# Optimization experiments

Measured on AMD Instinct MI355X. Metric: run time of the kernel, lower is better.

## Reference

```python
import jax, jax.numpy as jnp
import numpy as np

N_NODES = 100000
N_EDGES = 1600000
IN_CH = 64
HID = 64
N_GRAPHS = 64


def _sage_conv(x, src, dst, Wl, bl, Wr, n_nodes):
    # PyG SAGEConv (aggr='mean'): out = lin_l(mean_{j in N(i)} x_j) + lin_r(x_i)
    msg = x[src]                                            # [E, d] gather
    agg = jax.ops.segment_sum(msg, dst, num_segments=n_nodes)
    cnt = jax.ops.segment_sum(jnp.ones((src.shape[0],), x.dtype), dst,
                              num_segments=n_nodes)
    agg = agg / jnp.maximum(cnt, 1.0)[:, None]
    return agg @ Wl + bl + x @ Wr


def setup_inputs() -> dict:
    key = jax.random.key(0)
    ks = jax.random.split(key, 16)
    x = jax.random.normal(ks[0], (N_NODES, IN_CH), jnp.float32)
    edge_index = jax.random.randint(ks[1], (2, N_EDGES), 0, N_NODES, jnp.int64)
    batch = jnp.sort(jax.random.randint(ks[2], (N_NODES,), 0, N_GRAPHS, jnp.int64))

    def glorot(k, fan_in, fan_out):
        s = jnp.sqrt(2.0 / (fan_in + fan_out))
        return jax.random.normal(k, (fan_in, fan_out), jnp.float32) * s

    params = {
        'W1l': glorot(ks[3], IN_CH, HID), 'b1': jnp.zeros((HID,), jnp.float32),
        'W1r': glorot(ks[4], IN_CH, HID),
        'W2l': glorot(ks[5], HID, HID), 'b2': jnp.zeros((HID,), jnp.float32),
        'W2r': glorot(ks[6], HID, HID),
        'W3l': glorot(ks[7], HID, HID), 'b3': jnp.zeros((HID,), jnp.float32),
        'W3r': glorot(ks[8], HID, HID),
        'Wc1': glorot(ks[9], HID, HID // 2), 'bc1': jnp.zeros((HID // 2,), jnp.float32),
        'Wc2': glorot(ks[10], HID // 2, 2), 'bc2': jnp.zeros((2,), jnp.float32),
    }
    return {'x': x, 'edge_index': edge_index, 'batch': batch, **params}


def reference(x, edge_index, batch,
              W1l, b1, W1r, W2l, b2, W2r, W3l, b3, W3r,
              Wc1, bc1, Wc2, bc2):
    src, dst = edge_index[0], edge_index[1]
    n = x.shape[0]
    h = jax.nn.relu(_sage_conv(x, src, dst, W1l, b1, W1r, n))   # dropout = identity (eval)
    h = jax.nn.relu(_sage_conv(h, src, dst, W2l, b2, W2r, n))
    h = jax.nn.relu(_sage_conv(h, src, dst, W3l, b3, W3r, n))
    # global mean pool over graphs
    sums = jax.ops.segment_sum(h, batch, num_segments=N_GRAPHS)
    cnts = jax.ops.segment_sum(jnp.ones((n,), h.dtype), batch, num_segments=N_GRAPHS)
    g = sums / jnp.maximum(cnts, 1.0)[:, None]                  # [G, HID]
    # MLP head (dropout = identity at eval)
    return jax.nn.relu(g @ Wc1 + bc1) @ Wc2 + bc2               # [G, 2]
```

## Files before the change

kernel.cpp:

```cpp
#include <hip/hip_runtime.h>
#include <hip/hip_bf16.h>
#include <hip/hip_fp16.h>

typedef unsigned int u32;
typedef unsigned short u16;
typedef _Float16 f16x8 __attribute__((ext_vector_type(8)));
typedef float f32x4 __attribute__((ext_vector_type(4)));

#define NBLK1 512
#define CVTBLK 256
#define MMBLK 256

__device__ __forceinline__ u16 f2h(float f) { return __half_as_ushort(__float2half(f)); }
__device__ __forceinline__ u32 packh2(float a, float b) {
    return (u32)f2h(a) | ((u32)f2h(b) << 16);
}

__device__ __forceinline__ int gidx(const void* p, long long i, int w64) {
    if (w64) return (int)((const long long*)p)[i];
    return ((const int*)p)[i];
}

__device__ __forceinline__ int detect_w64(const int* edge_words, int E, int tid, int* sh) {
    if (tid == 0) *sh = 0;
    __syncthreads();
    const long long totalWords = 2LL * E;
    const long long step = totalWords / 256;
    long long w = ((long long)tid * step) | 1;
    int nz = (w < totalWords) ? edge_words[w] : 0;
    if (nz) atomicOr(sh, 1);
    __syncthreads();
    return (*sh) ? 0 : 1;
}

__global__ void __launch_bounds__(256) fused_hist_cvt(
        const void* __restrict__ edge, int* __restrict__ flag, u32* __restrict__ ticket,
        u32* __restrict__ HG, int E, int n, int nb1,
        const float* __restrict__ X, u16* __restrict__ Xh) {
    if (blockIdx.x < NBLK1) {
        __shared__ u32 h[256];
        __shared__ int shnz;
        const int tid = threadIdx.x;
        h[tid] = 0;
        const int w64 = detect_w64((const int*)edge, E, tid, &shnz);
        if (blockIdx.x == 0 && tid == 0) { flag[0] = w64; ticket[0] = 0; }
        __syncthreads();
        const int chunk = (E + NBLK1 - 1) / NBLK1;
        const int s = blockIdx.x * chunk;
        const int e = min(s + chunk, E);
        for (int i = s + tid; i < e; i += 256) {
            int d = gidx(edge, (long long)E + i, w64);
            if ((unsigned)d >= (unsigned)n) d = 0;
            atomicAdd(&h[d >> 9], 1);
        }
        __syncthreads();
        for (int b = tid; b < nb1; b += 256) HG[b * NBLK1 + blockIdx.x] = h[b];
        return;
    }
    const long long total4 = (long long)n * 16;
    const long long stride = (long long)CVTBLK * 256;
    long long i = (long long)(blockIdx.x - NBLK1) * 256 + threadIdx.x;
    const float4* X4 = (const float4*)X;
    uint2* O = (uint2*)Xh;
    for (; i < total4; i += stride) {
        float4 v = X4[i];
        uint2 o;
        o.x = packh2(v.x, v.y);
        o.y = packh2(v.z, v.w);
        O[i] = o;
    }
}

__global__ void scanAB(u32* __restrict__ HG, u32* __restrict__ blockSums,
                       u32* __restrict__ SB, u32* __restrict__ ticket, int n) {
    __shared__ u32 ts[256];
    __shared__ int isLast;
    const int ITEMS = 8;
    const int tid = threadIdx.x;
    int base = blockIdx.x * 2048 + tid * ITEMS;
    u32 v[ITEMS];
    u32 sum = 0;
#pragma unroll
    for (int i = 0; i < ITEMS; ++i) {
        int idx = base + i;
        v[i] = (idx < n) ? HG[idx] : 0;
        sum += v[i];
    }
    ts[tid] = sum;
    __syncthreads();
    u32 incl = sum;
    for (int d = 1; d < 256; d <<= 1) {
        u32 y = 0;
        if (tid >= d) y = ts[tid - d];
        __syncthreads();
        incl += y;
        ts[tid] = incl;
        __syncthreads();
    }
    u32 run = incl - sum;
#pragma unroll
    for (int i = 0; i < ITEMS; ++i) {
        int idx = base + i;
        if (idx < n) HG[idx] = run;
        run += v[i];
    }
    if (tid == 255) {
        atomicExch(&blockSums[blockIdx.x], incl);
        __threadfence();
        u32 t = atomicAdd(&ticket[0], 1u);
        isLast = (t == gridDim.x - 1);
    }
    __syncthreads();
    if (!isLast) return;
    const int nb = gridDim.x;
    u32 bv = (tid < nb) ? atomicAdd(&blockSums[tid], 0u) : 0;
    ts[tid] = bv;
    __syncthreads();
    u32 bincl = bv;
    for (int d = 1; d < 256; d <<= 1) {
        u32 y = 0;
        if (tid >= d) y = ts[tid - d];
        __syncthreads();
        bincl += y;
        ts[tid] = bincl;
        __syncthreads();
    }
    if (tid < nb) SB[tid] = bincl - bv;
}

__global__ void __launch_bounds__(256) p1_scatter(const void* __restrict__ edge,
                                                  const int* __restrict__ flag,
                                                  const u32* __restrict__ HG,
                                                  const u32* __restrict__ SB,
                                                  u32* __restrict__ P, int E, int n, int nb1) {
    __shared__ u32 base[256];
    __shared__ u32 cur[256];
    const int tid = threadIdx.x;
    cur[tid] = 0;
    for (int b = tid; b < nb1; b += 256) {
        int i = b * NBLK1 + blockIdx.x;
        base[b] = HG[i] + SB[i >> 11];
    }
    __syncthreads();
    const int w64 = flag[0];
    const int chunk = (E + NBLK1 - 1) / NBLK1;
    const int s = blockIdx.x * chunk;
    const int e = min(s + chunk, E);
    for (int i = s + tid; i < e; i += 256) {
        int d = gidx(edge, (long long)E + i, w64);
        if ((unsigned)d >= (unsigned)n) d = 0;
        int sv = gidx(edge, i, w64);
        if ((unsigned)sv >= (unsigned)n) sv = 0;
        const int b1 = d >> 9;
        u32 r = atomicAdd(&cur[b1], 1);
        P[base[b1] + r] = (u32)sv | ((u32)(d & 511) << 17);
    }
}

__global__ void __launch_bounds__(512) p2_kernel(const u32* __restrict__ P,
                                                 const u32* __restrict__ HG,
                                                 const u32* __restrict__ SB,
                                                 u32* __restrict__ offs,
                                                 int* __restrict__ ss,
                                                 float* __restrict__ pool,
                                                 int E, int n, int nb1) {
    __shared__ u32 h2[512];
    __shared__ u32 ts[512];
    const int tid = threadIdx.x;
    const int b = blockIdx.x;
    if (b == 0)
        for (int i = tid; i < 4096; i += 512) pool[i] = 0.f;
    const int i0 = b * NBLK1;
    const int bs = (int)(HG[i0] + SB[i0 >> 11]);
    int be;
    if (b + 1 < nb1) {
        const int i1 = (b + 1) * NBLK1;
        be = (int)(HG[i1] + SB[i1 >> 11]);
    } else be = E;
    h2[tid] = 0;
    __syncthreads();
    for (int i = bs + tid; i < be; i += 512) atomicAdd(&h2[(P[i] >> 17) & 511], 1);
    __syncthreads();
    u32 v = h2[tid];
    ts[tid] = v;
    __syncthreads();
    u32 incl = v;
    for (int d = 1; d < 512; d <<= 1) {
        u32 y = 0;
        if (tid >= d) y = ts[tid - d];
        __syncthreads();
        incl += y;
        ts[tid] = incl;
        __syncthreads();
    }
    u32 run = incl - v;
    h2[tid] = run;
    const int node0 = b * 512 + tid;
    if (node0 < n) offs[node0] = bs + run;
    if (b == 0 && tid == 0) offs[n] = (u32)E;
    __syncthreads();
    for (int i = bs + tid; i < be; i += 512) {
        u32 p = P[i];
        u32 r = atomicAdd(&h2[(p >> 17) & 511], 1);
        ss[bs + r] = (int)(p & 0x1FFFFu);
    }
}

__global__ void __launch_bounds__(256, 8) agg_kernel(
        const u16* __restrict__ G, const u32* __restrict__ offs,
        const int* __restrict__ ss, u16* __restrict__ M, int n) {
    const int lane = threadIdx.x & 63;
    const int quad = lane >> 4;
    const int m16 = lane & 15;
    const int ntiles = (n + 15) >> 4;
    const int nwaves = gridDim.x * 4;
    for (int tile = blockIdx.x * 4 + (threadIdx.x >> 6); tile < ntiles; tile += nwaves) {
        const int nodeBase = tile << 4;
        const int node_m = nodeBase + m16;
        const int valid = node_m < n;
        const int nodeA = valid ? node_m : n - 1;
        const u32 o0 = offs[nodeA];
        const int deg = valid ? (int)(offs[nodeA + 1] - o0) : 0;
        const int* sp = ss + o0;
        f16x8 s0, s1;
#pragma unroll
        for (int j = 0; j < 8; ++j) { s0[j] = (_Float16)0; s1[j] = (_Float16)0; }
        int e = 0;
        for (; e + 4 <= deg; e += 4) {
            const int iA = sp[e], iB = sp[e + 1], iC = sp[e + 2], iD = sp[e + 3];
            const f16x8* pA = (const f16x8*)(G + ((size_t)iA << 6)) + quad;
            const f16x8* pB = (const f16x8*)(G + ((size_t)iB << 6)) + quad;
            const f16x8* pC = (const f16x8*)(G + ((size_t)iC << 6)) + quad;
            const f16x8* pD = (const f16x8*)(G + ((size_t)iD << 6)) + quad;
            f16x8 a0 = pA[0], a1 = pA[4];
            f16x8 b0 = pB[0], b1 = pB[4];
            f16x8 c0 = pC[0], c1 = pC[4];
            f16x8 d0 = pD[0], d1 = pD[4];
            s0 += a0; s1 += a1;
            s0 += b0; s1 += b1;
            s0 += c0; s1 += c1;
            s0 += d0; s1 += d1;
        }
        for (; e < deg; ++e) {
            const int iA = sp[e];
            const f16x8* pA = (const f16x8*)(G + ((size_t)iA << 6)) + quad;
            s0 += pA[0]; s1 += pA[4];
        }
        const float rdf = deg > 0 ? 1.f / (float)deg : 0.f;
        const _Float16 hrd = (_Float16)rdf;
#pragma unroll
        for (int j = 0; j < 8; ++j) { s0[j] *= hrd; s1[j] *= hrd; }
        if (valid) {
            *(f16x8*)(M + (size_t)node_m * 64 + quad * 8) = s0;
            *(f16x8*)(M + (size_t)node_m * 64 + 32 + quad * 8) = s1;
        }
    }
}

__global__ void __launch_bounds__(256) mm_fused(
        const u16* __restrict__ M, const u16* __restrict__ G,
        const float* __restrict__ Wl, const float* __restrict__ Wr,
        const float* __restrict__ Bv,
        u16* __restrict__ Hout, float* __restrict__ pool,
        const void* __restrict__ batch, const int* __restrict__ flag,
        int n, int mode) {
    const int lane = threadIdx.x & 63;
    const int quad = lane >> 4;
    const int m16 = lane & 15;
    f16x8 bl[2][4], br[2][4];
#pragma unroll
    for (int kh = 0; kh < 2; ++kh)
#pragma unroll
        for (int t = 0; t < 4; ++t)
#pragma unroll
            for (int j = 0; j < 8; ++j) {
                int k = kh * 32 + quad * 8 + j;
                int c = t * 16 + m16;
                bl[kh][t][j] = (_Float16)Wl[k * 64 + c];
                br[kh][t][j] = (_Float16)Wr[k * 64 + c];
            }
    float bias_t[4];
#pragma unroll
    for (int t = 0; t < 4; ++t) bias_t[t] = Bv[t * 16 + m16];
    const int w64 = mode ? flag[0] : 0;

    const int ntiles = (n + 15) >> 4;
    const int nwaves = gridDim.x * 4;
    for (int tile = blockIdx.x * 4 + (threadIdx.x >> 6); tile < ntiles; tile += nwaves) {
        const int nodeBase = tile << 4;
        const int node_m = nodeBase + m16;
        const int nodeA = node_m < n ? node_m : n - 1;
        const f16x8 am0 = *(const f16x8*)(M + (size_t)nodeA * 64 + quad * 8);
        const f16x8 am1 = *(const f16x8*)(M + (size_t)nodeA * 64 + 32 + quad * 8);
        const f16x8 as0 = *(const f16x8*)(G + (size_t)nodeA * 64 + quad * 8);
        const f16x8 as1 = *(const f16x8*)(G + (size_t)nodeA * 64 + 32 + quad * 8);
        f32x4 c[4];
#pragma unroll
        for (int t = 0; t < 4; ++t) {
            f32x4 acc = {bias_t[t], bias_t[t], bias_t[t], bias_t[t]};
            acc = __builtin_amdgcn_mfma_f32_16x16x32_f16(am0, bl[0][t], acc, 0, 0, 0);
            acc = __builtin_amdgcn_mfma_f32_16x16x32_f16(am1, bl[1][t], acc, 0, 0, 0);
            acc = __builtin_amdgcn_mfma_f32_16x16x32_f16(as0, br[0][t], acc, 0, 0, 0);
            acc = __builtin_amdgcn_mfma_f32_16x16x32_f16(as1, br[1][t], acc, 0, 0, 0);
            c[t] = acc;
        }
        if (mode == 0) {
#pragma unroll
            for (int rg = 0; rg < 4; ++rg) {
                const int node = nodeBase + quad * 4 + rg;
                if (node < n) {
#pragma unroll
                    for (int t = 0; t < 4; ++t)
                        Hout[(size_t)node * 64 + t * 16 + m16] = f2h(fmaxf(c[t][rg], 0.f));
                }
            }
        } else {
            float v[4][4];
#pragma unroll
            for (int t = 0; t < 4; ++t)
#pragma unroll
                for (int rg = 0; rg < 4; ++rg) v[t][rg] = fmaxf(c[t][rg], 0.f);
            const int lastN = nodeBase + 15 < n ? nodeBase + 15 : n - 1;
            const int g0 = gidx(batch, nodeBase, w64) & 63;
            const int g1 = gidx(batch, lastN, w64) & 63;
            if (nodeBase + 15 < n && g0 == g1) {
#pragma unroll
                for (int t = 0; t < 4; ++t) {
                    float cs = v[t][0] + v[t][1] + v[t][2] + v[t][3];
                    cs += __shfl_xor(cs, 16, 64);
                    cs += __shfl_xor(cs, 32, 64);
                    if (quad == 0) atomicAdd(&pool[g0 * 64 + t * 16 + m16], cs);
                }
            } else {
#pragma unroll
                for (int rg = 0; rg < 4; ++rg) {
                    const int node = nodeBase + quad * 4 + rg;
                    if (node < n) {
                        const int g = gidx(batch, node, w64) & 63;
#pragma unroll
                        for (int t = 0; t < 4; ++t)
                            atomicAdd(&pool[g * 64 + t * 16 + m16], v[t][rg]);
                    }
                }
            }
        }
    }
}

__global__ void head_kernel(const float* __restrict__ pool, const void* __restrict__ batch,
                            const int* __restrict__ flag,
                            const float* __restrict__ Wc1, const float* __restrict__ bc1,
                            const float* __restrict__ Wc2, const float* __restrict__ bc2,
                            float* __restrict__ out, int n) {
    __shared__ float gm[64 * 64];
    __shared__ float am[64 * 32];
    __shared__ int cnts[64];
    const int tid = threadIdx.x;
    const int w64 = flag[0];
    if (tid < 64) {
        int lo = 0, hi = n;
        while (lo < hi) { int mid = (lo + hi) >> 1; if (gidx(batch, mid, w64) < tid) lo = mid + 1; else hi = mid; }
        int lo2 = 0, hi2 = n;
        int v2 = tid + 1;
        while (lo2 < hi2) { int mid = (lo2 + hi2) >> 1; if (gidx(batch, mid, w64) < v2) lo2 = mid + 1; else hi2 = mid; }
        cnts[tid] = lo2 - lo;
    }
    __syncthreads();
    for (int i = tid; i < 4096; i += 256) {
        int g = i >> 6;
        float c = (float)(cnts[g] > 0 ? cnts[g] : 1);
        gm[i] = pool[i] / c;
    }
    __syncthreads();
    for (int i = tid; i < 64 * 32; i += 256) {
        int g = i >> 5, j = i & 31;
        float acc = bc1[j];
        for (int k = 0; k < 64; ++k) acc += gm[g * 64 + k] * Wc1[k * 32 + j];
        am[i] = acc > 0.f ? acc : 0.f;
    }
    __syncthreads();
    if (tid < 128) {
        int g = tid >> 1, o = tid & 1;
        float acc = bc2[o];
        for (int j = 0; j < 32; ++j) acc += am[g * 32 + j] * Wc2[j * 2 + o];
        out[tid] = acc;
    }
}

extern "C" void kernel_launch(void* const* d_in, const int* in_sizes, int n_in,
                              void* d_out, int out_size, void* d_ws, size_t ws_size,
                              hipStream_t stream) {
    const float* x   = (const float*)d_in[0];
    const void* edge = d_in[1];
    const void* batch = d_in[2];
    const float* W1l = (const float*)d_in[3];
    const float* b1  = (const float*)d_in[4];
    const float* W1r = (const float*)d_in[5];
    const float* W2l = (const float*)d_in[6];
    const float* b2  = (const float*)d_in[7];
    const float* W2r = (const float*)d_in[8];
    const float* W3l = (const float*)d_in[9];
    const float* b3  = (const float*)d_in[10];
    const float* W3r = (const float*)d_in[11];
    const float* Wc1 = (const float*)d_in[12];
    const float* bc1 = (const float*)d_in[13];
    const float* Wc2 = (const float*)d_in[14];
    const float* bc2 = (const float*)d_in[15];

    const int n = in_sizes[0] / 64;
    const int E = in_sizes[1] / 2;
    const int nb1 = (n + 511) >> 9;
    const int NS = nb1 * NBLK1;

    char* w = (char*)d_ws;
    size_t o = 0;
    auto take = [&](size_t bytes) -> void* {
        void* p = w + o;
        o = (o + bytes + 511) & ~(size_t)511;
        return p;
    };
    int* flag      = (int*)take(sizeof(int));
    u32* ticket    = (u32*)take(2 * sizeof(u32));
    u32* offs      = (u32*)take((size_t)(n + 1) * sizeof(u32));
    u32* HG        = (u32*)take((size_t)(NS + 1) * sizeof(u32));
    u32* blockSums = (u32*)take(256 * sizeof(u32));
    u32* SB        = (u32*)take(256 * sizeof(u32));
    u32* P         = (u32*)take((size_t)E * sizeof(u32));
    int* ss        = (int*)take((size_t)E * sizeof(int));
    u16* Xh        = (u16*)take((size_t)n * 64 * sizeof(u16));
    u16* HA        = (u16*)take((size_t)n * 64 * sizeof(u16));
    u16* HB        = (u16*)take((size_t)n * 64 * sizeof(u16));
    u16* M         = (u16*)take((size_t)n * 64 * sizeof(u16));
    float* pool    = (float*)take(64 * 64 * sizeof(float));

    fused_hist_cvt<<<NBLK1 + CVTBLK, 256, 0, stream>>>(edge, flag, ticket, HG, E, n, nb1,
                                                       x, Xh);
    const int nbScan = (NS + 2047) / 2048;
    scanAB<<<nbScan, 256, 0, stream>>>(HG, blockSums, SB, ticket, NS);
    p1_scatter<<<NBLK1, 256, 0, stream>>>(edge, flag, HG, SB, P, E, n, nb1);
    p2_kernel<<<nb1, 512, 0, stream>>>(P, HG, SB, offs, ss, pool, E, n, nb1);

    const int ntiles = (n + 15) >> 4;
    const int AGGBLK = (ntiles + 3) >> 2;
    agg_kernel<<<AGGBLK, 256, 0, stream>>>(Xh, offs, ss, M, n);
    mm_fused<<<MMBLK, 256, 0, stream>>>(M, Xh, W1l, W1r, b1, HA, nullptr, batch, flag, n, 0);
    agg_kernel<<<AGGBLK, 256, 0, stream>>>(HA, offs, ss, M, n);
    mm_fused<<<MMBLK, 256, 0, stream>>>(M, HA, W2l, W2r, b2, HB, nullptr, batch, flag, n, 0);
    agg_kernel<<<AGGBLK, 256, 0, stream>>>(HB, offs, ss, M, n);
    mm_fused<<<MMBLK, 256, 0, stream>>>(M, HB, W3l, W3r, b3, nullptr, pool, batch, flag, n, 1);

    head_kernel<<<1, 256, 0, stream>>>(pool, batch, flag, Wc1, bc1, Wc2, bc2,
                                       (float*)d_out, n);
}
```

Before: 302.1 us.

## Split aggregation into feature slices with edge-parallel lanes and fp32 accumulation

The mean-aggregation kernel is restructured. Each block now handles one of eight 8-channel feature slices, and each node gets four lanes that split its edges among themselves, combining partial sums through xor shuffles. Neighbor indices are prefetched one step ahead and accumulation moves from fp16 to fp32. The grid becomes a fixed persistent size of 8×256 blocks. The aim is better load balance across nodes of differing degree and more parallel gathers in flight. The cost is that each node's index list is read eight times, and each gather is a 16-byte row fragment instead of a wider contiguous load.

```diff
diff --git a/kernel.cpp b/kernel.cpp
--- a/kernel.cpp
+++ b/kernel.cpp
@@ -10,6 +10,7 @@
 #define NBLK1 512
 #define CVTBLK 256
 #define MMBLK 256
+#define AGGBPS 256
 
 __device__ __forceinline__ u16 f2h(float f) { return __half_as_ushort(__float2half(f)); }
 __device__ __forceinline__ u32 packh2(float a, float b) {
@@ -206,53 +207,50 @@
     }
 }
 
-__global__ void __launch_bounds__(256, 8) agg_kernel(
+__global__ void __launch_bounds__(256) agg_kernel(
         const u16* __restrict__ G, const u32* __restrict__ offs,
         const int* __restrict__ ss, u16* __restrict__ M, int n) {
+    const int slice = blockIdx.x & 7;
+    const int blk = blockIdx.x >> 3;
+    const int nblkS = gridDim.x >> 3;
     const int lane = threadIdx.x & 63;
-    const int quad = lane >> 4;
-    const int m16 = lane & 15;
+    const int nsub = lane >> 2;
+    const int e4 = lane & 3;
+
     const int ntiles = (n + 15) >> 4;
-    const int nwaves = gridDim.x * 4;
-    for (int tile = blockIdx.x * 4 + (threadIdx.x >> 6); tile < ntiles; tile += nwaves) {
-        const int nodeBase = tile << 4;
-        const int node_m = nodeBase + m16;
+    const int wavesPerSlice = nblkS * 4;
+    for (int tile = blk * 4 + (threadIdx.x >> 6); tile < ntiles; tile += wavesPerSlice) {
+        const int node_m = (tile << 4) + nsub;
         const int valid = node_m < n;
         const int nodeA = valid ? node_m : n - 1;
         const u32 o0 = offs[nodeA];
         const int deg = valid ? (int)(offs[nodeA + 1] - o0) : 0;
         const int* sp = ss + o0;
-        f16x8 s0, s1;
-#pragma unroll
-        for (int j = 0; j < 8; ++j) { s0[j] = (_Float16)0; s1[j] = (_Float16)0; }
-        int e = 0;
-        for (; e + 4 <= deg; e += 4) {
-            const int iA = sp[e], iB = sp[e + 1], iC = sp[e + 2], iD = sp[e + 3];
-            const f16x8* pA = (const f16x8*)(G + ((size_t)iA << 6)) + quad;
-            const f16x8* pB = (const f16x8*)(G + ((size_t)iB << 6)) + quad;
-            const f16x8* pC = (const f16x8*)(G + ((size_t)iC << 6)) + quad;
-            const f16x8* pD = (const f16x8*)(G + ((size_t)iD << 6)) + quad;
-            f16x8 a0 = pA[0], a1 = pA[4];
-            f16x8 b0 = pB[0], b1 = pB[4];
-            f16x8 c0 = pC[0], c1 = pC[4];
-            f16x8 d0 = pD[0], d1 = pD[4];
-            s0 += a0; s1 += a1;
-            s0 += b0; s1 += b1;
-            s0 += c0; s1 += c1;
-            s0 += d0; s1 += d1;
-        }
-        for (; e < deg; ++e) {
-            const int iA = sp[e];
-            const f16x8* pA = (const f16x8*)(G + ((size_t)iA << 6)) + quad;
-            s0 += pA[0]; s1 += pA[4];
-        }
-        const float rdf = deg > 0 ? 1.f / (float)deg : 0.f;
-        const _Float16 hrd = (_Float16)rdf;
-#pragma unroll
-        for (int j = 0; j < 8; ++j) { s0[j] *= hrd; s1[j] *= hrd; }
-        if (valid) {
-            *(f16x8*)(M + (size_t)node_m * 64 + quad * 8) = s0;
-            *(f16x8*)(M + (size_t)node_m * 64 + 32 + quad * 8) = s1;
+        float acc[8];
+#pragma unroll
+        for (int j = 0; j < 8; ++j) acc[j] = 0.f;
+        int nidx = (e4 < deg) ? sp[e4] : -1;
+        for (int e = 0; e < deg; e += 4) {
+            const int idx = nidx;
+            const int en = e + 4;
+            nidx = (en + e4 < deg) ? sp[en + e4] : -1;
+            if (idx >= 0) {
+                const f16x8 r = *(const f16x8*)(G + ((size_t)idx << 6) + (slice << 3));
+#pragma unroll
+                for (int j = 0; j < 8; ++j) acc[j] += (float)r[j];
+            }
+        }
+#pragma unroll
+        for (int j = 0; j < 8; ++j) {
+            acc[j] += __shfl_xor(acc[j], 1, 64);
+            acc[j] += __shfl_xor(acc[j], 2, 64);
+        }
+        if (e4 == 0 && valid) {
+            const float rdf = deg > 0 ? 1.f / (float)deg : 0.f;
+            f16x8 o;
+#pragma unroll
+            for (int j = 0; j < 8; ++j) o[j] = (_Float16)(acc[j] * rdf);
+            *(f16x8*)(M + ((size_t)node_m << 6) + (slice << 3)) = o;
         }
     }
 }
@@ -440,8 +438,7 @@
     p1_scatter<<<NBLK1, 256, 0, stream>>>(edge, flag, HG, SB, P, E, n, nb1);
     p2_kernel<<<nb1, 512, 0, stream>>>(P, HG, SB, offs, ss, pool, E, n, nb1);
 
-    const int ntiles = (n + 15) >> 4;
-    const int AGGBLK = (ntiles + 3) >> 2;
+    const int AGGBLK = 8 * AGGBPS;
     agg_kernel<<<AGGBLK, 256, 0, stream>>>(Xh, offs, ss, M, n);
     mm_fused<<<MMBLK, 256, 0, stream>>>(M, Xh, W1l, W1r, b1, HA, nullptr, batch, flag, n, 0);
     agg_kernel<<<AGGBLK, 256, 0, stream>>>(HA, offs, ss, M, n);
```

Result: slower. 747.2 us (+147.4%).

## Split aggregation feature halves across waves and fuse head into last mm block

Applied to the files above, without the earlier changes.

The aggregation kernel now gives each node tile to two waves, each summing one 32-channel half, using a fixed grid of 2048 blocks with a grid-stride loop. This raises the number of independent gathers in flight per node, at the cost of reading the neighbor index list twice. The MLP head is folded into the final mm_fused launch: the last block to finish, found with an atomic ticket, reads the pool and computes the output, which removes one kernel launch. The pool is read back with atomic adds of zero so the last block sees every other block's writes.

```diff
diff --git a/kernel.cpp b/kernel.cpp
--- a/kernel.cpp
+++ b/kernel.cpp
@@ -10,6 +10,7 @@
 #define NBLK1 512
 #define CVTBLK 256
 #define MMBLK 256
+#define AGGBLK 2048
 
 __device__ __forceinline__ u16 f2h(float f) { return __half_as_ushort(__float2half(f)); }
 __device__ __forceinline__ u32 packh2(float a, float b) {
@@ -43,7 +44,7 @@
         const int tid = threadIdx.x;
         h[tid] = 0;
         const int w64 = detect_w64((const int*)edge, E, tid, &shnz);
-        if (blockIdx.x == 0 && tid == 0) { flag[0] = w64; ticket[0] = 0; }
+        if (blockIdx.x == 0 && tid == 0) { flag[0] = w64; ticket[0] = 0; ticket[1] = 0; }
         __syncthreads();
         const int chunk = (E + NBLK1 - 1) / NBLK1;
         const int s = blockIdx.x * chunk;
@@ -212,48 +213,37 @@
     const int lane = threadIdx.x & 63;
     const int quad = lane >> 4;
     const int m16 = lane & 15;
+    const int gw = blockIdx.x * 4 + (threadIdx.x >> 6);
+    const int half = gw & 1;
+    const int cb = half * 32 + quad * 8;
     const int ntiles = (n + 15) >> 4;
-    const int nwaves = gridDim.x * 4;
-    for (int tile = blockIdx.x * 4 + (threadIdx.x >> 6); tile < ntiles; tile += nwaves) {
-        const int nodeBase = tile << 4;
-        const int node_m = nodeBase + m16;
+    const int stride = (gridDim.x * 4) >> 1;
+    for (int tile = gw >> 1; tile < ntiles; tile += stride) {
+        const int node_m = (tile << 4) + m16;
         const int valid = node_m < n;
         const int nodeA = valid ? node_m : n - 1;
         const u32 o0 = offs[nodeA];
         const int deg = valid ? (int)(offs[nodeA + 1] - o0) : 0;
         const int* sp = ss + o0;
-        f16x8 s0, s1;
-#pragma unroll
-        for (int j = 0; j < 8; ++j) { s0[j] = (_Float16)0; s1[j] = (_Float16)0; }
+        f16x8 s;
+#pragma unroll
+        for (int j = 0; j < 8; ++j) s[j] = (_Float16)0;
         int e = 0;
         for (; e + 4 <= deg; e += 4) {
             const int iA = sp[e], iB = sp[e + 1], iC = sp[e + 2], iD = sp[e + 3];
-            const f16x8* pA = (const f16x8*)(G + ((size_t)iA << 6)) + quad;
-            const f16x8* pB = (const f16x8*)(G + ((size_t)iB << 6)) + quad;
-            const f16x8* pC = (const f16x8*)(G + ((size_t)iC << 6)) + quad;
-            const f16x8* pD = (const f16x8*)(G + ((size_t)iD << 6)) + quad;
-            f16x8 a0 = pA[0], a1 = pA[4];
-            f16x8 b0 = pB[0], b1 = pB[4];
-            f16x8 c0 = pC[0], c1 = pC[4];
-            f16x8 d0 = pD[0], d1 = pD[4];
-            s0 += a0; s1 += a1;
-            s0 += b0; s1 += b1;
-            s0 += c0; s1 += c1;
-            s0 += d0; s1 += d1;
+            f16x8 a = *(const f16x8*)(G + ((size_t)iA << 6) + cb);
+            f16x8 b = *(const f16x8*)(G + ((size_t)iB << 6) + cb);
+            f16x8 c = *(const f16x8*)(G + ((size_t)iC << 6) + cb);
+            f16x8 d = *(const f16x8*)(G + ((size_t)iD << 6) + cb);
+            s += a; s += b; s += c; s += d;
         }
-        for (; e < deg; ++e) {
-            const int iA = sp[e];
-            const f16x8* pA = (const f16x8*)(G + ((size_t)iA << 6)) + quad;
-            s0 += pA[0]; s1 += pA[4];
-        }
+        for (; e < deg; ++e)
+            s += *(const f16x8*)(G + ((size_t)(sp[e]) << 6) + cb);
         const float rdf = deg > 0 ? 1.f / (float)deg : 0.f;
         const _Float16 hrd = (_Float16)rdf;
 #pragma unroll
-        for (int j = 0; j < 8; ++j) { s0[j] *= hrd; s1[j] *= hrd; }
-        if (valid) {
-            *(f16x8*)(M + (size_t)node_m * 64 + quad * 8) = s0;
-            *(f16x8*)(M + (size_t)node_m * 64 + 32 + quad * 8) = s1;
-        }
+        for (int j = 0; j < 8; ++j) s[j] *= hrd;
+        if (valid) *(f16x8*)(M + ((size_t)node_m << 6) + cb) = s;
     }
 }
 
@@ -263,6 +253,10 @@
         const float* __restrict__ Bv,
         u16* __restrict__ Hout, float* __restrict__ pool,
         const void* __restrict__ batch, const int* __restrict__ flag,
+        u32* __restrict__ ticket,
+        const float* __restrict__ Wc1, const float* __restrict__ bc1,
+        const float* __restrict__ Wc2, const float* __restrict__ bc2,
+        float* __restrict__ out,
         int n, int mode) {
     const int lane = threadIdx.x & 63;
     const int quad = lane >> 4;
@@ -345,18 +339,18 @@
             }
         }
     }
-}
-
-__global__ void head_kernel(const float* __restrict__ pool, const void* __restrict__ batch,
-                            const int* __restrict__ flag,
-                            const float* __restrict__ Wc1, const float* __restrict__ bc1,
-                            const float* __restrict__ Wc2, const float* __restrict__ bc2,
-                            float* __restrict__ out, int n) {
+    if (mode == 0) return;
+
     __shared__ float gm[64 * 64];
     __shared__ float am[64 * 32];
     __shared__ int cnts[64];
+    __shared__ int isLast;
     const int tid = threadIdx.x;
-    const int w64 = flag[0];
+    __threadfence();
+    if (tid == 0) isLast = (atomicAdd(&ticket[1], 1u) == gridDim.x - 1);
+    __syncthreads();
+    if (!isLast) return;
+    __threadfence();
     if (tid < 64) {
         int lo = 0, hi = n;
         while (lo < hi) { int mid = (lo + hi) >> 1; if (gidx(batch, mid, w64) < tid) lo = mid + 1; else hi = mid; }
@@ -369,7 +363,7 @@
     for (int i = tid; i < 4096; i += 256) {
         int g = i >> 6;
         float c = (float)(cnts[g] > 0 ? cnts[g] : 1);
-        gm[i] = pool[i] / c;
+        gm[i] = atomicAdd(&pool[i], 0.f) / c;
     }
     __syncthreads();
     for (int i = tid; i < 64 * 32; i += 256) {
@@ -440,15 +434,16 @@
     p1_scatter<<<NBLK1, 256, 0, stream>>>(edge, flag, HG, SB, P, E, n, nb1);
     p2_kernel<<<nb1, 512, 0, stream>>>(P, HG, SB, offs, ss, pool, E, n, nb1);
 
-    const int ntiles = (n + 15) >> 4;
-    const int AGGBLK = (ntiles + 3) >> 2;
     agg_kernel<<<AGGBLK, 256, 0, stream>>>(Xh, offs, ss, M, n);
-    mm_fused<<<MMBLK, 256, 0, stream>>>(M, Xh, W1l, W1r, b1, HA, nullptr, batch, flag, n, 0);
+    mm_fused<<<MMBLK, 256, 0, stream>>>(M, Xh, W1l, W1r, b1, HA, nullptr, batch, flag,
+                                        ticket, nullptr, nullptr, nullptr, nullptr,
+                                        nullptr, n, 0);
     agg_kernel<<<AGGBLK, 256, 0, stream>>>(HA, offs, ss, M, n);
-    mm_fused<<<MMBLK, 256, 0, stream>>>(M, HA, W2l, W2r, b2, HB, nullptr, batch, flag, n, 0);
+    mm_fused<<<MMBLK, 256, 0, stream>>>(M, HA, W2l, W2r, b2, HB, nullptr, batch, flag,
+                                        ticket, nullptr, nullptr, nullptr, nullptr,
+                                        nullptr, n, 0);
     agg_kernel<<<AGGBLK, 256, 0, stream>>>(HB, offs, ss, M, n);
-    mm_fused<<<MMBLK, 256, 0, stream>>>(M, HB, W3l, W3r, b3, nullptr, pool, batch, flag, n, 1);
-
-    head_kernel<<<1, 256, 0, stream>>>(pool, batch, flag, Wc1, bc1, Wc2, bc2,
-                                       (float*)d_out, n);
-}
+    mm_fused<<<MMBLK, 256, 0, stream>>>(M, HB, W3l, W3r, b3, nullptr, pool, batch, flag,
+                                        ticket, Wc1, bc1, Wc2, bc2,
+                                        (float*)d_out, n, 1);
+}
```

Result: slower. 323.4 us (+7.1%).
